# Performance work log

Measured on AMD Instinct MI355X. Metric: run time of the kernel, lower is better.

## Reference

```python
import jax, jax.numpy as jnp
import numpy as np

D_MODEL = 1024
N_HEADS = 16
D_K = 64  # per-head dim and the scaling denominator used by the module
NEG = -1e9  # stand-in for -inf in masked_fill (rows are never fully masked)


def setup_inputs() -> dict:
    key = jax.random.key(0)
    ks = jax.random.split(key, 8)
    B, M, N = 2, 2048, 2048
    q = jax.random.normal(ks[0], (B, M, D_MODEL), dtype=jnp.float32)
    k = jax.random.normal(ks[1], (B, N, D_MODEL), dtype=jnp.float32)
    v = jax.random.normal(ks[2], (B, N, D_MODEL), dtype=jnp.float32)
    mask = jax.random.randint(ks[3], (B, M, N), 0, 2).astype(jnp.bool_)
    # xavier_uniform for square [d,d] weights: limit = sqrt(6/(d+d))
    lim = float(np.sqrt(6.0 / (D_MODEL + D_MODEL)))
    Wq = jax.random.uniform(ks[4], (D_MODEL, D_MODEL), jnp.float32, -lim, lim)
    Wk = jax.random.uniform(ks[5], (D_MODEL, D_MODEL), jnp.float32, -lim, lim)
    Wv = jax.random.uniform(ks[6], (D_MODEL, D_MODEL), jnp.float32, -lim, lim)
    Wo = jax.random.uniform(ks[7], (D_MODEL, D_MODEL), jnp.float32, -lim, lim)
    return {"q": q, "k": k, "v": v, "mask": mask,
            "Wq": Wq, "Wk": Wk, "Wv": Wv, "Wo": Wo}


def _split_heads(x):
    # (B, S, D) -> (B, H, S, Dh); the torch split/cat-on-batch trick is
    # mathematically identical to this standard head reshape.
    B, S, _ = x.shape
    return x.reshape(B, S, N_HEADS, D_K).transpose(0, 2, 1, 3)


def reference(q, k, v, mask, Wq, Wk, Wv, Wo):
    qw = _split_heads(q @ Wq.T)  # (B,H,M,Dh)
    kw = _split_heads(k @ Wk.T)  # (B,H,N,Dh)
    vw = _split_heads(v @ Wv.T)  # (B,H,N,Dh)
    scores = jnp.einsum('bhmd,bhnd->bhmn', qw, kw)
    scores = jnp.where(mask[:, None, :, :], NEG, scores)
    attn = jax.nn.softmax(scores / jnp.sqrt(jnp.float32(D_K)), axis=-1)
    ctx = jnp.einsum('bhmn,bhnd->bhmd', attn, vw)
    B, _, M, _ = ctx.shape
    ctx = ctx.transpose(0, 2, 1, 3).reshape(B, M, D_MODEL)
    return ctx @ Wo.T
```

## Files before the change

### kernel.cpp

```cpp
#include <hip/hip_runtime.h>
#include <hip/hip_bf16.h>
#include <stdint.h>
#include <string.h>

#define SEQ   2048
#define DM    1024
#define NH    16
#define NB    2

typedef __attribute__((ext_vector_type(8))) short bf16x8;
typedef __attribute__((ext_vector_type(4))) float f32x4;
typedef unsigned short u16;
typedef unsigned int   u32;

__device__ __forceinline__ u16 f2bf(float f) {
    u32 u = __float_as_uint(f);
    u += 0x7FFF + ((u >> 16) & 1);
    return (u16)(u >> 16);
}
__device__ __forceinline__ u32 pk2bf(float a, float b) {
    __hip_bfloat162 p = __float22bfloat162_rn(make_float2(a, b));
    u32 u; memcpy(&u, &p, 4); return u;
}
__device__ __forceinline__ float fexp2(float x) {
#if __has_builtin(__builtin_amdgcn_exp2f)
    return __builtin_amdgcn_exp2f(x);
#else
    return exp2f(x);
#endif
}
__device__ __forceinline__ void gl_lds16(const void* g, void* l) {
    __builtin_amdgcn_global_load_lds(
        (const __attribute__((address_space(1))) u32*)g,
        (__attribute__((address_space(3))) u32*)l, 16, 0, 0);
}

struct CvtArgs {
    const float* s[7];
    u16* d[7];
    float scale[7];
    int start[8];
};
__global__ __launch_bounds__(256) void cvt_kernel(CvtArgs a) {
    int bid = blockIdx.x;
    int seg = 0;
#pragma unroll
    for (int i = 1; i < 7; ++i) if (bid >= a.start[i]) seg = i;
    float sc = a.scale[seg];
    size_t base = (size_t)(bid - a.start[seg]) * 2048 + threadIdx.x * 8;
    const float4* s4 = (const float4*)(a.s[seg] + base);
    float4 x = s4[0], y = s4[1];
    u32 r[4];
    r[0] = pk2bf(x.x*sc, x.y*sc); r[1] = pk2bf(x.z*sc, x.w*sc);
    r[2] = pk2bf(y.x*sc, y.y*sc); r[3] = pk2bf(y.z*sc, y.w*sc);
    *(uint4*)(a.d[seg] + base) = *(uint4*)r;
}

__global__ void maskpack_kernel(const int* __restrict__ mask,
                                unsigned int* __restrict__ bits) {
    int gid = blockIdx.x * 256 + threadIdx.x;
    int m = mask[gid];
    unsigned long long bal = __ballot(m != 0);
    int lane = threadIdx.x & 63;
    if (lane == 0)       bits[gid >> 5] = (u32)(bal & 0xFFFFFFFFull);
    else if (lane == 32) bits[gid >> 5] = (u32)(bal >> 32);
}

template<int RT>
__device__ __forceinline__ void gemm_body(const u16* __restrict__ A,
                                          const u16* __restrict__ Bm,
                                          void* __restrict__ Y,
                                          int rtile, int ctile, int mode,
                                          u16* sA, u16* sB) {
    const int tid  = threadIdx.x;
    const int wv   = tid >> 6, lane = tid & 63;
    const int quad = lane >> 4, ln = lane & 15;
    const int wr   = wv >> 1,  wc  = wv & 1;

    const int lr = lane >> 3;
    const int lc = (lane & 7) ^ lr;
    const u16* gA[RT]; const u16* gB[4];
    u16 *lA[RT], *lB[4];
#pragma unroll
    for (int s = 0; s < RT; ++s) {
        int seg = wv * RT + s;
        gA[s] = A + (size_t)(rtile * (RT*32) + seg*8 + lr) * 1024 + lc*8;
        lA[s] = sA + seg * 512;
    }
#pragma unroll
    for (int s = 0; s < 4; ++s) {
        int seg = wv * 4 + s;
        gB[s] = Bm + (size_t)(ctile * 128 + seg*8 + lr) * 1024 + lc*8;
        lB[s] = sB + seg * 512;
    }

    f32x4 acc[RT][4];
#pragma unroll
    for (int i = 0; i < RT; ++i)
#pragma unroll
        for (int j = 0; j < 4; ++j) acc[i][j] = (f32x4){0.f,0.f,0.f,0.f};

    const int c0 = (quad ^ (ln & 7)) * 8;

    for (int kt = 0; kt < 16; ++kt) {
        if (kt) __syncthreads();
#pragma unroll
        for (int s = 0; s < RT; ++s) gl_lds16(gA[s] + kt*64, lA[s]);
#pragma unroll
        for (int s = 0; s < 4; ++s) gl_lds16(gB[s] + kt*64, lB[s]);
        __syncthreads();

        bf16x8 a0[RT], a1[RT], b0[4], b1[4];
#pragma unroll
        for (int rt = 0; rt < RT; ++rt) {
            const u16* p = sA + (wr*(RT*16) + rt*16 + ln) * 64;
            a0[rt] = *(const bf16x8*)(p + c0);
            a1[rt] = *(const bf16x8*)(p + (c0 ^ 32));
        }
#pragma unroll
        for (int ct = 0; ct < 4; ++ct) {
            const u16* p = sB + (wc*64 + ct*16 + ln) * 64;
            b0[ct] = *(const bf16x8*)(p + c0);
            b1[ct] = *(const bf16x8*)(p + (c0 ^ 32));
        }
#pragma unroll
        for (int rt = 0; rt < RT; ++rt)
#pragma unroll
            for (int ct = 0; ct < 4; ++ct) {
                acc[rt][ct] = __builtin_amdgcn_mfma_f32_16x16x32_bf16(
                    a0[rt], b0[ct], acc[rt][ct], 0, 0, 0);
                acc[rt][ct] = __builtin_amdgcn_mfma_f32_16x16x32_bf16(
                    a1[rt], b1[ct], acc[rt][ct], 0, 0, 0);
            }
    }

#pragma unroll
    for (int rt = 0; rt < RT; ++rt) {
#pragma unroll
        for (int ct = 0; ct < 4; ++ct) {
#pragma unroll
            for (int i = 0; i < 4; ++i) {
                int R = rtile*(RT*32) + wr*(RT*16) + rt*16 + quad*4 + i;
                int C = ctile*128 + wc*64 + ct*16 + ln;
                float val = acc[rt][ct][i];
                if (mode == 0) {
                    int b = R >> 11, s = R & 2047, h = C >> 6, d = C & 63;
                    ((u16*)Y)[((size_t)((b*NH + h) * SEQ + s) << 6) + d] = f2bf(val);
                } else if (mode == 1) {
                    int h = R >> 6, d = R & 63, b = C >> 11, n = C & 2047;
                    ((u16*)Y)[((size_t)((b*NH + h) * 64 + d) << 11) + n] = f2bf(val);
                } else {
                    ((float*)Y)[(size_t)R * 1024 + C] = val;
                }
            }
        }
    }
}

struct QKVArgs { const u16* A[3]; const u16* B[3]; u16* Y[3]; };

__global__ __launch_bounds__(256) void gemm_qkv(QKVArgs g) {
    __shared__ u16 sA[128 * 64];
    __shared__ u16 sB[128 * 64];
    int z = blockIdx.z;
    if (z == 2)
        gemm_body<4>(g.A[2], g.B[2], g.Y[2], blockIdx.y, blockIdx.x, 1, sA, sB);
    else
        gemm_body<4>(g.A[z], g.B[z], g.Y[z], blockIdx.x, blockIdx.y, 0, sA, sB);
}

__global__ __launch_bounds__(256) void gemm_out(const u16* __restrict__ A,
                                                const u16* __restrict__ Bm,
                                                float* __restrict__ Y) {
    __shared__ u16 sA[64 * 64];
    __shared__ u16 sB[128 * 64];
    gemm_body<2>(A, Bm, Y, blockIdx.x, blockIdx.y, 2, sA, sB);
}

__global__ __launch_bounds__(256) void attn_kernel(
    const u16* __restrict__ qw,
    const u16* __restrict__ kw,
    const u16* __restrict__ vt,
    const u32* __restrict__ mbits,
    u16* __restrict__ ctx) {

    constexpr int PST = 68;
    __shared__ u16 sK[64 * 64];
    __shared__ u16 sV[64 * 64];
    __shared__ u16 sP[4 * 16 * PST];

    const int mtile = blockIdx.x;
    const int bh    = blockIdx.y;
    const int b     = bh >> 4;
    const int tid   = threadIdx.x;
    const int wv    = tid >> 6, lane = tid & 63;
    const int quad  = lane >> 4, ln = lane & 15;
    const int m0    = mtile * 64;

    const size_t hbase = (size_t)bh * SEQ * 64;

    bf16x8 qf[2];
    {
        const u16* qp = qw + hbase + (size_t)(m0 + wv*16 + ln) * 64 + quad*8;
        qf[0] = *(const bf16x8*)(qp);
        qf[1] = *(const bf16x8*)(qp + 32);
    }

    f32x4 o[4], lsum;
#pragma unroll
    for (int i = 0; i < 4; ++i) o[i] = (f32x4){0.f,0.f,0.f,0.f};
    lsum = (f32x4){0.f,0.f,0.f,0.f};

    bf16x8 ones;
#pragma unroll
    for (int i = 0; i < 8; ++i) ones[i] = (short)0x3F80;

    const u32* mrow[4];
#pragma unroll
    for (int i = 0; i < 4; ++i)
        mrow[i] = mbits + (size_t)(b * SEQ + m0 + wv*16 + quad*4 + i) * 64;

    const u32 mlo = 1u << ln;
    const u32 mhi = 1u << (ln + 16);

    const int lr = lane >> 3;
    const int lc = (lane & 7) ^ lr;
    const u16* gK[2]; const u16* gV[2];
    u16 *lK[2], *lV[2];
#pragma unroll
    for (int s = 0; s < 2; ++s) {
        int seg = s * 4 + wv;
        gK[s] = kw + hbase + (size_t)(seg*8 + lr) * 64 + lc*8;
        gV[s] = vt + hbase + (size_t)(seg*8 + lr) * SEQ + lc*8;
        lK[s] = sK + seg * 512;
        lV[s] = sV + seg * 512;
    }

    const int c0 = (quad ^ (ln & 7)) * 8;
    u16* sPw = sP + wv * 16 * PST;

    for (int nt = 0; nt < SEQ / 64; ++nt) {
        __syncthreads();
#pragma unroll
        for (int s = 0; s < 2; ++s) {
            gl_lds16(gK[s] + (size_t)nt * 4096, lK[s]);
            gl_lds16(gV[s] + nt * 64, lV[s]);
        }
        uint2 ww[4];
#pragma unroll
        for (int i = 0; i < 4; ++i)
            ww[i] = *(const uint2*)(mrow[i] + nt * 2);
        __syncthreads();

        f32x4 s4[4];
#pragma unroll
        for (int ct = 0; ct < 4; ++ct) {
            const u16* kp = sK + (ct*16 + ln) * 64;
            bf16x8 k0 = *(const bf16x8*)(kp + c0);
            bf16x8 k1 = *(const bf16x8*)(kp + (c0 ^ 32));
            f32x4 z = (f32x4){0.f, 0.f, 0.f, 0.f};
            z = __builtin_amdgcn_mfma_f32_16x16x32_bf16(qf[0], k0, z, 0, 0, 0);
            z = __builtin_amdgcn_mfma_f32_16x16x32_bf16(qf[1], k1, z, 0, 0, 0);
            s4[ct] = z;
        }

#pragma unroll
        for (int ct = 0; ct < 4; ++ct) {
            const u32 mb = (ct & 1) ? mhi : mlo;
            float p0, p1;
#pragma unroll
            for (int ii = 0; ii < 4; ii += 2) {
                u32 w0 = (ct & 2) ? ww[ii].y   : ww[ii].x;
                u32 w1 = (ct & 2) ? ww[ii+1].y : ww[ii+1].x;
                p0 = fexp2((w0 & mb) ? -1e9f : s4[ct][ii]);
                p1 = fexp2((w1 & mb) ? -1e9f : s4[ct][ii+1]);
                u32 u = pk2bf(p0, p1);
                sPw[(quad*4 + ii)     * PST + ct*16 + ln] = (u16)u;
                sPw[(quad*4 + ii + 1) * PST + ct*16 + ln] = (u16)(u >> 16);
            }
        }
        __syncthreads();

        bf16x8 pf0 = *(const bf16x8*)(sPw + ln*PST + quad*8);
        bf16x8 pf1 = *(const bf16x8*)(sPw + ln*PST + 32 + quad*8);
        lsum = __builtin_amdgcn_mfma_f32_16x16x32_bf16(pf0, ones, lsum, 0, 0, 0);
        lsum = __builtin_amdgcn_mfma_f32_16x16x32_bf16(pf1, ones, lsum, 0, 0, 0);
#pragma unroll
        for (int ct = 0; ct < 4; ++ct) {
            const u16* vp = sV + (ct*16 + ln) * 64;
            bf16x8 v0 = *(const bf16x8*)(vp + c0);
            bf16x8 v1 = *(const bf16x8*)(vp + (c0 ^ 32));
            o[ct] = __builtin_amdgcn_mfma_f32_16x16x32_bf16(pf0, v0, o[ct], 0, 0, 0);
            o[ct] = __builtin_amdgcn_mfma_f32_16x16x32_bf16(pf1, v1, o[ct], 0, 0, 0);
        }
    }

#pragma unroll
    for (int i = 0; i < 4; ++i) {
        float inv = 1.f / lsum[i];
        int m = m0 + wv*16 + quad*4 + i;
        size_t base = ((size_t)(b * SEQ + m) << 10) + (bh & 15) * 64;
#pragma unroll
        for (int ct = 0; ct < 4; ++ct)
            ctx[base + ct*16 + ln] = f2bf(o[ct][i] * inv);
    }
}

extern "C" void kernel_launch(void* const* d_in, const int* in_sizes, int n_in,
                              void* d_out, int out_size, void* d_ws, size_t ws_size,
                              hipStream_t stream) {
    const float* q    = (const float*)d_in[0];
    const float* k    = (const float*)d_in[1];
    const float* v    = (const float*)d_in[2];
    const int*   mask = (const int*)d_in[3];
    const float* Wq   = (const float*)d_in[4];
    const float* Wk   = (const float*)d_in[5];
    const float* Wv   = (const float*)d_in[6];
    const float* Wo   = (const float*)d_in[7];
    float* out = (float*)d_out;

    char* ws = (char*)d_ws;
    const size_t SZH = (size_t)NB * SEQ * DM * 2;
    const size_t SZW = (size_t)DM * DM * 2;
    u16* qw   = (u16*)(ws);
    u16* kw   = (u16*)(ws + SZH);
    u16* vt   = (u16*)(ws + 2*SZH);
    u16* ctx  = (u16*)(ws + 3*SZH);
    u16* vb   = ctx;
    u32* mbits= (u32*)(ws + 4*SZH);
    u16* qb   = (u16*)(ws + 4*SZH + (1u<<20));
    u16* kb   = (u16*)(ws + 4*SZH + (1u<<20) + SZH);
    u16* Wqb  = (u16*)(ws + 4*SZH + (1u<<20) + 2*SZH);
    u16* Wkb  = (u16*)((char*)Wqb + SZW);
    u16* Wvb  = (u16*)((char*)Wqb + 2*SZW);
    u16* Wob  = (u16*)((char*)Wqb + 3*SZW);

    const float CSC = 0.18033688011112042f;

    CvtArgs ca;
    ca.s[0]=q;  ca.d[0]=qb;  ca.scale[0]=1.f;
    ca.s[1]=k;  ca.d[1]=kb;  ca.scale[1]=1.f;
    ca.s[2]=v;  ca.d[2]=vb;  ca.scale[2]=1.f;
    ca.s[3]=Wq; ca.d[3]=Wqb; ca.scale[3]=CSC;
    ca.s[4]=Wk; ca.d[4]=Wkb; ca.scale[4]=1.f;
    ca.s[5]=Wv; ca.d[5]=Wvb; ca.scale[5]=1.f;
    ca.s[6]=Wo; ca.d[6]=Wob; ca.scale[6]=1.f;
    int st[8] = {0, 2048, 4096, 6144, 6656, 7168, 7680, 8192};
    for (int i = 0; i < 8; ++i) ca.start[i] = st[i];
    cvt_kernel<<<dim3(8192), dim3(256), 0, stream>>>(ca);

    maskpack_kernel<<<dim3(NB*SEQ*SEQ/256), dim3(256), 0, stream>>>(mask, mbits);

    QKVArgs ga;
    ga.A[0]=qb;  ga.B[0]=Wqb; ga.Y[0]=qw;
    ga.A[1]=kb;  ga.B[1]=Wkb; ga.Y[1]=kw;
    ga.A[2]=Wvb; ga.B[2]=vb;  ga.Y[2]=vt;
    gemm_qkv<<<dim3(32, 8, 3), dim3(256), 0, stream>>>(ga);

    attn_kernel<<<dim3(SEQ/64, NB*NH), dim3(256), 0, stream>>>(qw, kw, vt, mbits, ctx);

    gemm_out<<<dim3(64, 8), dim3(256), 0, stream>>>(ctx, Wob, out);
}
```

Baseline: 277.0 us.

## Double-buffer LDS loads in GEMMs and attention, widen attention tile to 128 rows

The GEMM body now uses K-steps of 32 with two LDS buffers, so the next tile's global-to-LDS copy is issued before the MFMAs on the current one, and the swizzle is adapted to the narrower rows. The attention kernel double-buffers K/V tiles and mask words and gives each wave two 16-row query tiles (128 rows per block). This reuses each K/V load across twice as many rows and removes one barrier per iteration. In exchange it uses more LDS and registers, halves the attention grid, and relies on a single barrier per iteration staying correct with the prefetch writing the other buffer.

```diff
diff --git a/kernel.cpp b/kernel.cpp
--- a/kernel.cpp
+++ b/kernel.cpp
@@ -72,25 +72,28 @@
                                           void* __restrict__ Y,
                                           int rtile, int ctile, int mode,
                                           u16* sA, u16* sB) {
+    constexpr int ABUF = RT * 32 * 32;
+    constexpr int BBUF = 128 * 32;
     const int tid  = threadIdx.x;
     const int wv   = tid >> 6, lane = tid & 63;
     const int quad = lane >> 4, ln = lane & 15;
     const int wr   = wv >> 1,  wc  = wv & 1;
 
-    const int lr = lane >> 3;
-    const int lc = (lane & 7) ^ lr;
-    const u16* gA[RT]; const u16* gB[4];
-    u16 *lA[RT], *lB[4];
-#pragma unroll
-    for (int s = 0; s < RT; ++s) {
-        int seg = wv * RT + s;
-        gA[s] = A + (size_t)(rtile * (RT*32) + seg*8 + lr) * 1024 + lc*8;
+    const int lr4 = lane >> 2;
+    const int lcc = ((lane & 3) ^ ((lane >> 3) & 3)) * 8;
+
+    const u16* gA[RT/2]; u16* lA[RT/2];
+#pragma unroll
+    for (int s = 0; s < RT/2; ++s) {
+        int seg = wv * (RT/2) + s;
+        gA[s] = A + (size_t)(rtile * (RT*32) + seg*16 + lr4) * 1024 + lcc;
         lA[s] = sA + seg * 512;
     }
-#pragma unroll
-    for (int s = 0; s < 4; ++s) {
-        int seg = wv * 4 + s;
-        gB[s] = Bm + (size_t)(ctile * 128 + seg*8 + lr) * 1024 + lc*8;
+    const u16* gB[2]; u16* lB[2];
+#pragma unroll
+    for (int s = 0; s < 2; ++s) {
+        int seg = wv * 2 + s;
+        gB[s] = Bm + (size_t)(ctile * 128 + seg*16 + lr4) * 1024 + lcc;
         lB[s] = sB + seg * 512;
     }
 
@@ -100,38 +103,39 @@
 #pragma unroll
         for (int j = 0; j < 4; ++j) acc[i][j] = (f32x4){0.f,0.f,0.f,0.f};
 
-    const int c0 = (quad ^ (ln & 7)) * 8;
-
-    for (int kt = 0; kt < 16; ++kt) {
-        if (kt) __syncthreads();
-#pragma unroll
-        for (int s = 0; s < RT; ++s) gl_lds16(gA[s] + kt*64, lA[s]);
-#pragma unroll
-        for (int s = 0; s < 4; ++s) gl_lds16(gB[s] + kt*64, lB[s]);
+    const int c0 = (quad ^ ((ln >> 1) & 3)) * 8;
+
+#pragma unroll
+    for (int s = 0; s < RT/2; ++s) gl_lds16(gA[s], lA[s]);
+#pragma unroll
+    for (int s = 0; s < 2; ++s)    gl_lds16(gB[s], lB[s]);
+
+    for (int kt = 0; kt < 32; ++kt) {
         __syncthreads();
-
-        bf16x8 a0[RT], a1[RT], b0[4], b1[4];
-#pragma unroll
-        for (int rt = 0; rt < RT; ++rt) {
-            const u16* p = sA + (wr*(RT*16) + rt*16 + ln) * 64;
-            a0[rt] = *(const bf16x8*)(p + c0);
-            a1[rt] = *(const bf16x8*)(p + (c0 ^ 32));
-        }
-#pragma unroll
-        for (int ct = 0; ct < 4; ++ct) {
-            const u16* p = sB + (wc*64 + ct*16 + ln) * 64;
-            b0[ct] = *(const bf16x8*)(p + c0);
-            b1[ct] = *(const bf16x8*)(p + (c0 ^ 32));
-        }
+        if (kt < 31) {
+            int nb = (kt + 1) & 1;
+#pragma unroll
+            for (int s = 0; s < RT/2; ++s)
+                gl_lds16(gA[s] + (kt+1)*32, lA[s] + nb*ABUF);
+#pragma unroll
+            for (int s = 0; s < 2; ++s)
+                gl_lds16(gB[s] + (kt+1)*32, lB[s] + nb*BBUF);
+        }
+        const u16* sAb = sA + (kt & 1) * ABUF;
+        const u16* sBb = sB + (kt & 1) * BBUF;
+        bf16x8 af[RT], bfr[4];
 #pragma unroll
         for (int rt = 0; rt < RT; ++rt)
-#pragma unroll
-            for (int ct = 0; ct < 4; ++ct) {
+            af[rt] = *(const bf16x8*)(sAb + (wr*(RT*16) + rt*16 + ln) * 32 + c0);
+#pragma unroll
+        for (int ct = 0; ct < 4; ++ct)
+            bfr[ct] = *(const bf16x8*)(sBb + (wc*64 + ct*16 + ln) * 32 + c0);
+#pragma unroll
+        for (int rt = 0; rt < RT; ++rt)
+#pragma unroll
+            for (int ct = 0; ct < 4; ++ct)
                 acc[rt][ct] = __builtin_amdgcn_mfma_f32_16x16x32_bf16(
-                    a0[rt], b0[ct], acc[rt][ct], 0, 0, 0);
-                acc[rt][ct] = __builtin_amdgcn_mfma_f32_16x16x32_bf16(
-                    a1[rt], b1[ct], acc[rt][ct], 0, 0, 0);
-            }
+                    af[rt], bfr[ct], acc[rt][ct], 0, 0, 0);
     }
 
 #pragma unroll
@@ -160,8 +164,8 @@
 struct QKVArgs { const u16* A[3]; const u16* B[3]; u16* Y[3]; };
 
 __global__ __launch_bounds__(256) void gemm_qkv(QKVArgs g) {
-    __shared__ u16 sA[128 * 64];
-    __shared__ u16 sB[128 * 64];
+    __shared__ u16 sA[2 * 128 * 32];
+    __shared__ u16 sB[2 * 128 * 32];
     int z = blockIdx.z;
     if (z == 2)
         gemm_body<4>(g.A[2], g.B[2], g.Y[2], blockIdx.y, blockIdx.x, 1, sA, sB);
@@ -172,8 +176,8 @@
 __global__ __launch_bounds__(256) void gemm_out(const u16* __restrict__ A,
                                                 const u16* __restrict__ Bm,
                                                 float* __restrict__ Y) {
-    __shared__ u16 sA[64 * 64];
-    __shared__ u16 sB[128 * 64];
+    __shared__ u16 sA[2 * 64 * 32];
+    __shared__ u16 sB[2 * 128 * 32];
     gemm_body<2>(A, Bm, Y, blockIdx.x, blockIdx.y, 2, sA, sB);
 }
 
@@ -185,9 +189,9 @@
     u16* __restrict__ ctx) {
 
     constexpr int PST = 68;
-    __shared__ u16 sK[64 * 64];
-    __shared__ u16 sV[64 * 64];
-    __shared__ u16 sP[4 * 16 * PST];
+    __shared__ u16 sK[2 * 64 * 64];
+    __shared__ u16 sV[2 * 64 * 64];
+    __shared__ u16 sP[4 * 32 * PST];
 
     const int mtile = blockIdx.x;
     const int bh    = blockIdx.y;
@@ -195,31 +199,31 @@
     const int tid   = threadIdx.x;
     const int wv    = tid >> 6, lane = tid & 63;
     const int quad  = lane >> 4, ln = lane & 15;
-    const int m0    = mtile * 64;
+    const int m0    = mtile * 128;
 
     const size_t hbase = (size_t)bh * SEQ * 64;
 
-    bf16x8 qf[2];
-    {
-        const u16* qp = qw + hbase + (size_t)(m0 + wv*16 + ln) * 64 + quad*8;
-        qf[0] = *(const bf16x8*)(qp);
-        qf[1] = *(const bf16x8*)(qp + 32);
-    }
-
-    f32x4 o[4], lsum;
-#pragma unroll
-    for (int i = 0; i < 4; ++i) o[i] = (f32x4){0.f,0.f,0.f,0.f};
-    lsum = (f32x4){0.f,0.f,0.f,0.f};
+    bf16x8 qf[2][2];
+#pragma unroll
+    for (int mt = 0; mt < 2; ++mt) {
+        const u16* qp = qw + hbase + (size_t)(m0 + (wv*2+mt)*16 + ln) * 64 + quad*8;
+        qf[mt][0] = *(const bf16x8*)(qp);
+        qf[mt][1] = *(const bf16x8*)(qp + 32);
+    }
+
+    f32x4 o[2][4], lsum[2];
+#pragma unroll
+    for (int mt = 0; mt < 2; ++mt) {
+        lsum[mt] = (f32x4){0.f,0.f,0.f,0.f};
+#pragma unroll
+        for (int j = 0; j < 4; ++j) o[mt][j] = (f32x4){0.f,0.f,0.f,0.f};
+    }
 
     bf16x8 ones;
 #pragma unroll
     for (int i = 0; i < 8; ++i) ones[i] = (short)0x3F80;
 
-    const u32* mrow[4];
-#pragma unroll
-    for (int i = 0; i < 4; ++i)
-        mrow[i] = mbits + (size_t)(b * SEQ + m0 + wv*16 + quad*4 + i) * 64;
-
+    const u32* mbase = mbits + (size_t)(b * SEQ + m0 + wv*32 + quad*4) * 64;
     const u32 mlo = 1u << ln;
     const u32 mhi = 1u << (ln + 16);
 
@@ -237,73 +241,109 @@
     }
 
     const int c0 = (quad ^ (ln & 7)) * 8;
-    u16* sPw = sP + wv * 16 * PST;
+    u16* sPw = sP + wv * 32 * PST;
+
+#pragma unroll
+    for (int s = 0; s < 2; ++s) { gl_lds16(gK[s], lK[s]); gl_lds16(gV[s], lV[s]); }
+    uint2 wwA[2][4];
+#pragma unroll
+    for (int mt = 0; mt < 2; ++mt)
+#pragma unroll
+        for (int i = 0; i < 4; ++i)
+            wwA[mt][i] = *(const uint2*)(mbase + (mt*16 + i)*64);
 
     for (int nt = 0; nt < SEQ / 64; ++nt) {
         __syncthreads();
-#pragma unroll
-        for (int s = 0; s < 2; ++s) {
-            gl_lds16(gK[s] + (size_t)nt * 4096, lK[s]);
-            gl_lds16(gV[s] + nt * 64, lV[s]);
-        }
-        uint2 ww[4];
-#pragma unroll
-        for (int i = 0; i < 4; ++i)
-            ww[i] = *(const uint2*)(mrow[i] + nt * 2);
-        __syncthreads();
-
-        f32x4 s4[4];
+        uint2 wwB[2][4];
+        if (nt < SEQ/64 - 1) {
+            int nb = (nt + 1) & 1;
+#pragma unroll
+            for (int s = 0; s < 2; ++s) {
+                gl_lds16(gK[s] + (size_t)(nt+1) * 4096, lK[s] + nb*4096);
+                gl_lds16(gV[s] + (nt+1) * 64,           lV[s] + nb*4096);
+            }
+#pragma unroll
+            for (int mt = 0; mt < 2; ++mt)
+#pragma unroll
+                for (int i = 0; i < 4; ++i)
+                    wwB[mt][i] = *(const uint2*)(mbase + (mt*16 + i)*64 + (nt+1)*2);
+        }
+        const u16* sKb = sK + (nt & 1) * 4096;
+        const u16* sVb = sV + (nt & 1) * 4096;
+
+        f32x4 s4[2][4];
 #pragma unroll
         for (int ct = 0; ct < 4; ++ct) {
-            const u16* kp = sK + (ct*16 + ln) * 64;
+            const u16* kp = sKb + (ct*16 + ln) * 64;
             bf16x8 k0 = *(const bf16x8*)(kp + c0);
             bf16x8 k1 = *(const bf16x8*)(kp + (c0 ^ 32));
-            f32x4 z = (f32x4){0.f, 0.f, 0.f, 0.f};
-            z = __builtin_amdgcn_mfma_f32_16x16x32_bf16(qf[0], k0, z, 0, 0, 0);
-            z = __builtin_amdgcn_mfma_f32_16x16x32_bf16(qf[1], k1, z, 0, 0, 0);
-            s4[ct] = z;
-        }
-
+#pragma unroll
+            for (int mt = 0; mt < 2; ++mt) {
+                f32x4 z = (f32x4){0.f, 0.f, 0.f, 0.f};
+                z = __builtin_amdgcn_mfma_f32_16x16x32_bf16(qf[mt][0], k0, z, 0, 0, 0);
+                z = __builtin_amdgcn_mfma_f32_16x16x32_bf16(qf[mt][1], k1, z, 0, 0, 0);
+                s4[mt][ct] = z;
+            }
+        }
+
+#pragma unroll
+        for (int mt = 0; mt < 2; ++mt) {
+#pragma unroll
+            for (int ct = 0; ct < 4; ++ct) {
+                const u32 mb = (ct & 1) ? mhi : mlo;
+#pragma unroll
+                for (int ii = 0; ii < 4; ii += 2) {
+                    u32 w0 = (ct & 2) ? wwA[mt][ii].y   : wwA[mt][ii].x;
+                    u32 w1 = (ct & 2) ? wwA[mt][ii+1].y : wwA[mt][ii+1].x;
+                    float p0 = fexp2((w0 & mb) ? -1e9f : s4[mt][ct][ii]);
+                    float p1 = fexp2((w1 & mb) ? -1e9f : s4[mt][ct][ii+1]);
+                    u32 u = pk2bf(p0, p1);
+                    int row = mt*16 + quad*4 + ii;
+                    sPw[ row    * PST + ct*16 + ln] = (u16)u;
+                    sPw[(row+1) * PST + ct*16 + ln] = (u16)(u >> 16);
+                }
+            }
+        }
+
+        bf16x8 pf[2][2];
+#pragma unroll
+        for (int mt = 0; mt < 2; ++mt) {
+            const u16* pp = sPw + (mt*16 + ln) * PST;
+            pf[mt][0] = *(const bf16x8*)(pp + quad*8);
+            pf[mt][1] = *(const bf16x8*)(pp + 32 + quad*8);
+            lsum[mt] = __builtin_amdgcn_mfma_f32_16x16x32_bf16(pf[mt][0], ones, lsum[mt], 0, 0, 0);
+            lsum[mt] = __builtin_amdgcn_mfma_f32_16x16x32_bf16(pf[mt][1], ones, lsum[mt], 0, 0, 0);
+        }
 #pragma unroll
         for (int ct = 0; ct < 4; ++ct) {
-            const u32 mb = (ct & 1) ? mhi : mlo;
-            float p0, p1;
-#pragma unroll
-            for (int ii = 0; ii < 4; ii += 2) {
-                u32 w0 = (ct & 2) ? ww[ii].y   : ww[ii].x;
-                u32 w1 = (ct & 2) ? ww[ii+1].y : ww[ii+1].x;
-                p0 = fexp2((w0 & mb) ? -1e9f : s4[ct][ii]);
-                p1 = fexp2((w1 & mb) ? -1e9f : s4[ct][ii+1]);
-                u32 u = pk2bf(p0, p1);
-                sPw[(quad*4 + ii)     * PST + ct*16 + ln] = (u16)u;
-                sPw[(quad*4 + ii + 1) * PST + ct*16 + ln] = (u16)(u >> 16);
-            }
-        }
-        __syncthreads();
-
-        bf16x8 pf0 = *(const bf16x8*)(sPw + ln*PST + quad*8);
-        bf16x8 pf1 = *(const bf16x8*)(sPw + ln*PST + 32 + quad*8);
-        lsum = __builtin_amdgcn_mfma_f32_16x16x32_bf16(pf0, ones, lsum, 0, 0, 0);
-        lsum = __builtin_amdgcn_mfma_f32_16x16x32_bf16(pf1, ones, lsum, 0, 0, 0);
-#pragma unroll
-        for (int ct = 0; ct < 4; ++ct) {
-            const u16* vp = sV + (ct*16 + ln) * 64;
+            const u16* vp = sVb + (ct*16 + ln) * 64;
             bf16x8 v0 = *(const bf16x8*)(vp + c0);
             bf16x8 v1 = *(const bf16x8*)(vp + (c0 ^ 32));
-            o[ct] = __builtin_amdgcn_mfma_f32_16x16x32_bf16(pf0, v0, o[ct], 0, 0, 0);
-            o[ct] = __builtin_amdgcn_mfma_f32_16x16x32_bf16(pf1, v1, o[ct], 0, 0, 0);
-        }
-    }
-
-#pragma unroll
-    for (int i = 0; i < 4; ++i) {
-        float inv = 1.f / lsum[i];
-        int m = m0 + wv*16 + quad*4 + i;
-        size_t base = ((size_t)(b * SEQ + m) << 10) + (bh & 15) * 64;
-#pragma unroll
-        for (int ct = 0; ct < 4; ++ct)
-            ctx[base + ct*16 + ln] = f2bf(o[ct][i] * inv);
-    }
+#pragma unroll
+            for (int mt = 0; mt < 2; ++mt) {
+                o[mt][ct] = __builtin_amdgcn_mfma_f32_16x16x32_bf16(pf[mt][0], v0, o[mt][ct], 0, 0, 0);
+                o[mt][ct] = __builtin_amdgcn_mfma_f32_16x16x32_bf16(pf[mt][1], v1, o[mt][ct], 0, 0, 0);
+            }
+        }
+
+#pragma unroll
+        for (int mt = 0; mt < 2; ++mt)
+#pragma unroll
+            for (int i = 0; i < 4; ++i)
+                wwA[mt][i] = wwB[mt][i];
+    }
+
+#pragma unroll
+    for (int mt = 0; mt < 2; ++mt)
+#pragma unroll
+        for (int i = 0; i < 4; ++i) {
+            float inv = 1.f / lsum[mt][i];
+            int m = m0 + (wv*2+mt)*16 + quad*4 + i;
+            size_t base = ((size_t)(b * SEQ + m) << 10) + (bh & 15) * 64;
+#pragma unroll
+            for (int ct = 0; ct < 4; ++ct)
+                ctx[base + ct*16 + ln] = f2bf(o[mt][ct][i] * inv);
+        }
 }
 
 extern "C" void kernel_launch(void* const* d_in, const int* in_sizes, int n_in,
@@ -357,7 +397,7 @@
     ga.A[2]=Wvb; ga.B[2]=vb;  ga.Y[2]=vt;
     gemm_qkv<<<dim3(32, 8, 3), dim3(256), 0, stream>>>(ga);
 
-    attn_kernel<<<dim3(SEQ/64, NB*NH), dim3(256), 0, stream>>>(qw, kw, vt, mbits, ctx);
+    attn_kernel<<<dim3(SEQ/128, NB*NH), dim3(256), 0, stream>>>(qw, kw, vt, mbits, ctx);
 
     gemm_out<<<dim3(64, 8), dim3(256), 0, stream>>>(ctx, Wob, out);
 }
```

New measurement: 296.8 us. 1.07x slower.
